# Performance work log

Hardware: AMD Instinct MI355X
Metric: run time of the kernel (lower is better)

Reference implementation:

```python
import jax, jax.numpy as jnp
import numpy as np

N, E, IN, H, C, T = 50000, 800000, 128, 64, 64, 2
F1, FO1 = H, H // T   # conv1: per-tower in/out feats
F2, FO2 = H, C // T   # conv2
STD_EPS = 1e-5
BN_EPS = 1e-5


def setup_inputs() -> dict:
    key = jax.random.key(0)
    ks = jax.random.split(key, 12)
    rn = lambda k, s, sc=0.05: jax.random.normal(k, s, jnp.float32) * sc
    return {
        "x": jax.random.normal(ks[0], (N, IN), jnp.float32),
        "embed_W": rn(ks[1], (IN, H)),
        "embed_b": jnp.zeros((H,), jnp.float32),
        "pre_W1": rn(ks[2], (T, 2 * F1, F1)),
        "pre_b1": jnp.zeros((T, F1), jnp.float32),
        "post_W1": rn(ks[3], (T, 13 * F1, FO1)),
        "post_b1": jnp.zeros((T, FO1), jnp.float32),
        "lin_W1": rn(ks[4], (H, H)),
        "lin_b1": jnp.zeros((H,), jnp.float32),
        "bn_gamma": jnp.ones((H,), jnp.float32),
        "bn_beta": jnp.zeros((H,), jnp.float32),
        "pre_W2": rn(ks[5], (T, 2 * F2, F2)),
        "pre_b2": jnp.zeros((T, F2), jnp.float32),
        "post_W2": rn(ks[6], (T, 13 * F2, FO2)),
        "post_b2": jnp.zeros((T, FO2), jnp.float32),
        "lin_W2": rn(ks[7], (C, C)),
        "lin_b2": jnp.zeros((C,), jnp.float32),
        "src": jax.random.randint(ks[8], (E,), 0, N, jnp.int32),
        "dst": jax.random.randint(ks[9], (E,), 0, N, jnp.int32),
    }


def _pna_conv(h, src, dst, deg_raw, degc, avg_log, preW, preb, postW, postb, linW, linb):
    # h: [N, F] node feats; messages flow src -> dst, aggregated at dst.
    m = jnp.concatenate([h[dst], h[src]], axis=-1)            # [E, 2F]  (cat[x_i, x_j])
    m = jnp.einsum('ef,tfg->etg', m, preW) + preb[None]       # [E, T, F] per-tower pre-NN
    seg = lambda v: jax.ops.segment_sum(v, dst, num_segments=N)
    cnt = degc[:, None, None]                                 # clamped degree >= 1
    has = (deg_raw > 0)[:, None, None]
    mean = seg(m) / cnt                                       # [N, T, F]
    mean_sq = seg(m * m) / cnt
    mn = jnp.where(has, jax.ops.segment_min(m, dst, num_segments=N), 0.0)
    mx = jnp.where(has, jax.ops.segment_max(m, dst, num_segments=N), 0.0)
    std = jnp.sqrt(jax.nn.relu(mean_sq - mean * mean) + STD_EPS)
    agg = jnp.concatenate([mean, mn, mx, std], axis=-1)       # [N, T, 4F]
    ld = jnp.log(degc + 1.0)[:, None, None]
    out = jnp.concatenate([agg, agg * (ld / avg_log), agg * (avg_log / ld)], axis=-1)  # [N, T, 12F]
    F = h.shape[-1]
    out = jnp.concatenate([jnp.broadcast_to(h[:, None, :], (N, T, F)), out], axis=-1)  # [N, T, 13F]
    out = jnp.einsum('ntf,tfg->ntg', out, postW) + postb[None]  # [N, T, FO] per-tower post-NN
    return out.reshape(N, -1) @ linW + linb                    # final mixing Linear(out, out)


def reference(x, embed_W, embed_b, pre_W1, pre_b1, post_W1, post_b1, lin_W1, lin_b1,
              bn_gamma, bn_beta, pre_W2, pre_b2, post_W2, post_b2, lin_W2, lin_b2,
              src, dst):
    deg_raw = jax.ops.segment_sum(jnp.ones((E,), jnp.float32), dst, num_segments=N)
    degc = jnp.maximum(deg_raw, 1.0)
    avg_log = jnp.mean(jnp.log(deg_raw + 1.0))  # avg_deg['log'] from the graph's degrees
    h = x @ embed_W + embed_b
    h = _pna_conv(h, src, dst, deg_raw, degc, avg_log,
                  pre_W1, pre_b1, post_W1, post_b1, lin_W1, lin_b1)
    mu = jnp.mean(h, axis=0)
    var = jnp.mean((h - mu) ** 2, axis=0)
    h = bn_gamma * (h - mu) / jnp.sqrt(var + BN_EPS) + bn_beta
    h = jax.nn.relu(h)  # dropout is identity in eval mode
    return _pna_conv(h, src, dst, deg_raw, degc, avg_log,
                     pre_W2, pre_b2, post_W2, post_b2, lin_W2, lin_b2)
```

## Files before the change

### kernel.cpp

```cpp
#include <hip/hip_runtime.h>

#define N_NODES 50000
#define E_EDGES 800000
#define IN_F    128
#define H_F     64
#define STD_EPS 1e-5f
#define BN_EPS  1e-5f

__global__ __launch_bounds__(256) void k_hist(const int* __restrict__ dst,
                                              int* __restrict__ deg) {
  int e = blockIdx.x * 256 + threadIdx.x;
  if (e < E_EDGES) atomicAdd(&deg[dst[e]], 1);
}

__global__ __launch_bounds__(256) void k_sumlog(const int* __restrict__ deg,
                                                float* __restrict__ scalars) {
  __shared__ float red[256];
  int i = blockIdx.x * 256 + threadIdx.x;
  float v = 0.f;
  if (i < N_NODES) v = logf((float)deg[i] + 1.0f);
  red[threadIdx.x] = v; __syncthreads();
  for (int s = 128; s > 0; s >>= 1) {
    if (threadIdx.x < s) red[threadIdx.x] += red[threadIdx.x + s];
    __syncthreads();
  }
  if (threadIdx.x == 0) atomicAdd(&scalars[0], red[0]);
}

__global__ __launch_bounds__(256) void k_scan_part(const int* __restrict__ deg,
                                                   int* __restrict__ partials) {
  __shared__ int red[256];
  int base = blockIdx.x * 1024;
  int s = 0;
  for (int j = threadIdx.x; j < 1024; j += 256) {
    int i = base + j;
    if (i < N_NODES) s += deg[i];
  }
  red[threadIdx.x] = s; __syncthreads();
  for (int st = 128; st > 0; st >>= 1) {
    if (threadIdx.x < st) red[threadIdx.x] += red[threadIdx.x + st];
    __syncthreads();
  }
  if (threadIdx.x == 0) partials[blockIdx.x] = red[0];
}

__global__ void k_scan_mid(int* __restrict__ partials, int nblk,
                           float* __restrict__ scalars) {
  if (threadIdx.x == 0) {
    int run = 0;
    for (int b = 0; b < nblk; b++) { int v = partials[b]; partials[b] = run; run += v; }
    scalars[1] = scalars[0] / (float)N_NODES;
  }
}

__global__ __launch_bounds__(256) void k_scan_final(const int* __restrict__ deg,
                                                    const int* __restrict__ partials,
                                                    int* __restrict__ row_ptr,
                                                    int* __restrict__ cursor) {
  __shared__ int ts[256];
  int base = blockIdx.x * 1024 + threadIdx.x * 4;
  int d[4]; int s = 0;
#pragma unroll
  for (int j = 0; j < 4; j++) {
    int i = base + j;
    d[j] = (i < N_NODES) ? deg[i] : 0;
    s += d[j];
  }
  ts[threadIdx.x] = s; __syncthreads();
  for (int off = 1; off < 256; off <<= 1) {
    int t = (threadIdx.x >= off) ? ts[threadIdx.x - off] : 0;
    __syncthreads();
    ts[threadIdx.x] += t;
    __syncthreads();
  }
  int excl = (threadIdx.x > 0) ? ts[threadIdx.x - 1] : 0;
  int run = partials[blockIdx.x] + excl;
#pragma unroll
  for (int j = 0; j < 4; j++) {
    int i = base + j;
    if (i < N_NODES) { row_ptr[i] = run; cursor[i] = run; run += d[j]; }
  }
  if (blockIdx.x == 0 && threadIdx.x == 0) row_ptr[N_NODES] = E_EDGES;
}

__global__ __launch_bounds__(256) void k_scatter(const int* __restrict__ src,
                                                 const int* __restrict__ dst,
                                                 int* __restrict__ cursor,
                                                 int* __restrict__ csr_src) {
  int e = blockIdx.x * 256 + threadIdx.x;
  if (e < E_EDGES) {
    int d = dst[e];
    int p = atomicAdd(&cursor[d], 1);
    csr_src[p] = src[e];
  }
}

__global__ __launch_bounds__(256) void k_embed(const float* __restrict__ x,
                                               const float* __restrict__ W,
                                               const float* __restrict__ bias,
                                               float* __restrict__ h) {
  __shared__ float sW[IN_F * 64];
  __shared__ float sx[IN_F * 20];
  for (int i = threadIdx.x; i < IN_F * 64; i += 256) sW[i] = W[i];
  int j = threadIdx.x & 63, ng = threadIdx.x >> 6;
  float bj = bias[j];
  for (int grp = blockIdx.x; grp < N_NODES / 16; grp += gridDim.x) {
    int n0 = grp * 16;
    __syncthreads();
    for (int idx = threadIdx.x; idx < 16 * IN_F; idx += 256) {
      int nl = idx >> 7, k = idx & 127;
      sx[k * 20 + nl] = x[(size_t)(n0 + nl) * IN_F + k];
    }
    __syncthreads();
    float a0 = bj, a1 = bj, a2 = bj, a3 = bj;
    const float* xp = &sx[ng * 4];
#pragma unroll 4
    for (int k = 0; k < IN_F; k++) {
      float4 xv = *(const float4*)&xp[k * 20];
      float w = sW[k * 64 + j];
      a0 = fmaf(xv.x, w, a0); a1 = fmaf(xv.y, w, a1);
      a2 = fmaf(xv.z, w, a2); a3 = fmaf(xv.w, w, a3);
    }
    size_t ob = (size_t)(n0 + ng * 4) * 64 + j;
    h[ob] = a0; h[ob + 64] = a1; h[ob + 128] = a2; h[ob + 192] = a3;
  }
}

template <bool BN>
__global__ __launch_bounds__(256) void k_preab(const float* __restrict__ hin,
                                               const float* __restrict__ preW,
                                               const float* __restrict__ preb,
                                               const float* __restrict__ bnscale,
                                               const float* __restrict__ bnshift,
                                               float* __restrict__ h2out,
                                               float* __restrict__ hA,
                                               float* __restrict__ hB) {
  __shared__ float sW[128 * 64];
  __shared__ float sh[64 * 20];
  int t = blockIdx.x & 1;
  const float* Wsrc = preW + (size_t)t * 128 * 64;
  for (int i = threadIdx.x; i < 128 * 64; i += 256) sW[i] = Wsrc[i];
  int f = threadIdx.x & 63, ng = threadIdx.x >> 6;
  float pb = preb[t * 64 + f];
  const float* wA = &sW[f];
  const float* wB = &sW[64 * 64 + f];
  int nblk2 = gridDim.x >> 1;
  for (int grp = blockIdx.x >> 1; grp < N_NODES / 16; grp += nblk2) {
    int n0 = grp * 16;
    __syncthreads();
    for (int idx = threadIdx.x; idx < 16 * 64; idx += 256) {
      int nl = idx >> 6, k = idx & 63;
      float v = hin[(size_t)(n0 + nl) * 64 + k];
      if (BN) {
        v = fmaxf(fmaf(v, bnscale[k], bnshift[k]), 0.f);
        if (t == 0) h2out[(size_t)(n0 + nl) * 64 + k] = v;
      }
      sh[k * 20 + nl] = v;
    }
    __syncthreads();
    float a0 = pb, a1 = pb, a2 = pb, a3 = pb;
    float b0 = 0, b1 = 0, b2 = 0, b3 = 0;
    const float* hp = &sh[ng * 4];
#pragma unroll 4
    for (int k = 0; k < 64; k++) {
      float4 hv = *(const float4*)&hp[k * 20];
      float wa = wA[k * 64], wb = wB[k * 64];
      a0 = fmaf(hv.x, wa, a0); a1 = fmaf(hv.y, wa, a1);
      a2 = fmaf(hv.z, wa, a2); a3 = fmaf(hv.w, wa, a3);
      b0 = fmaf(hv.x, wb, b0); b1 = fmaf(hv.y, wb, b1);
      b2 = fmaf(hv.z, wb, b2); b3 = fmaf(hv.w, wb, b3);
    }
    size_t nb = (size_t)(n0 + ng * 4);
    int tf = t * 64 + f;
    hA[nb * 128 + tf] = a0;          hB[nb * 128 + tf] = b0;
    hA[(nb + 1) * 128 + tf] = a1;    hB[(nb + 1) * 128 + tf] = b1;
    hA[(nb + 2) * 128 + tf] = a2;    hB[(nb + 2) * 128 + tf] = b2;
    hA[(nb + 3) * 128 + tf] = a3;    hB[(nb + 3) * 128 + tf] = b3;
  }
}

__global__ __launch_bounds__(256, 6) void k_conv(const float* __restrict__ hA,
                                                 const float* __restrict__ hB,
                                                 const float* __restrict__ hskip,
                                                 const int* __restrict__ row_ptr,
                                                 const int* __restrict__ csr_src,
                                                 const float* __restrict__ postW,
                                                 const float* __restrict__ postb,
                                                 const float* __restrict__ linW,
                                                 const float* __restrict__ linb,
                                                 const float* __restrict__ scalars,
                                                 float* __restrict__ out) {
  __shared__ float sm[2 * 5 * 8 * 64];
  __shared__ float sAB[16];
  int w = threadIdx.x >> 6, lane = threadIdx.x & 63;
  int n0 = blockIdx.x * 8;
  int t = lane >> 5, fb = (lane & 31) * 2;
  int off = t * 64 + fb;
  float avg = scalars[1];

#pragma unroll 1
  for (int k = 0; k < 2; k++) {
    int nl = w * 2 + k;
    int n = n0 + nl;
    float2 a = *(const float2*)&hA[(size_t)n * 128 + off];
    int rp0 = __builtin_amdgcn_readfirstlane(row_ptr[n]);
    int rp1 = __builtin_amdgcn_readfirstlane(row_ptr[n + 1]);
    float sx0=0,sy0=0,qx0=0,qy0=0, sx1=0,sy1=0,qx1=0,qy1=0;
    float mnx0=INFINITY,mny0=INFINITY,mxx0=-INFINITY,mxy0=-INFINITY;
    float mnx1=INFINITY,mny1=INFINITY,mxx1=-INFINITY,mxy1=-INFINITY;
    int i = rp0;
    int end4 = rp0 + ((rp1 - rp0) & ~3);
    if (i < end4) {
      int s0 = csr_src[i], s1 = csr_src[i+1], s2 = csr_src[i+2], s3 = csr_src[i+3];
      while (true) {
        float2 v0 = *(const float2*)&hB[(size_t)s0 * 128 + off];
        float2 v1 = *(const float2*)&hB[(size_t)s1 * 128 + off];
        float2 v2 = *(const float2*)&hB[(size_t)s2 * 128 + off];
        float2 v3 = *(const float2*)&hB[(size_t)s3 * 128 + off];
        i += 4;
        bool more = (i < end4);
        if (more) { s0 = csr_src[i]; s1 = csr_src[i+1]; s2 = csr_src[i+2]; s3 = csr_src[i+3]; }
        float e0x = v0.x + a.x, e0y = v0.y + a.y;
        float e1x = v1.x + a.x, e1y = v1.y + a.y;
        float e2x = v2.x + a.x, e2y = v2.y + a.y;
        float e3x = v3.x + a.x, e3y = v3.y + a.y;
        sx0 += e0x; qx0 = fmaf(e0x,e0x,qx0); mnx0 = fminf(mnx0,e0x); mxx0 = fmaxf(mxx0,e0x);
        sy0 += e0y; qy0 = fmaf(e0y,e0y,qy0); mny0 = fminf(mny0,e0y); mxy0 = fmaxf(mxy0,e0y);
        sx1 += e1x; qx1 = fmaf(e1x,e1x,qx1); mnx1 = fminf(mnx1,e1x); mxx1 = fmaxf(mxx1,e1x);
        sy1 += e1y; qy1 = fmaf(e1y,e1y,qy1); mny1 = fminf(mny1,e1y); mxy1 = fmaxf(mxy1,e1y);
        sx0 += e2x; qx0 = fmaf(e2x,e2x,qx0); mnx0 = fminf(mnx0,e2x); mxx0 = fmaxf(mxx0,e2x);
        sy0 += e2y; qy0 = fmaf(e2y,e2y,qy0); mny0 = fminf(mny0,e2y); mxy0 = fmaxf(mxy0,e2y);
        sx1 += e3x; qx1 = fmaf(e3x,e3x,qx1); mnx1 = fminf(mnx1,e3x); mxx1 = fmaxf(mxx1,e3x);
        sy1 += e3y; qy1 = fmaf(e3y,e3y,qy1); mny1 = fminf(mny1,e3y); mxy1 = fmaxf(mxy1,e3y);
        if (!more) break;
      }
    }
    {
      int r = rp1 - i;
      if (r > 0) {
        int e1i = (r > 1) ? i + 1 : i;
        int e2i = (r > 2) ? i + 2 : i;
        int t0 = csr_src[i], t1 = csr_src[e1i], t2 = csr_src[e2i];
        float2 u0 = *(const float2*)&hB[(size_t)t0 * 128 + off];
        float2 u1 = *(const float2*)&hB[(size_t)t1 * 128 + off];
        float2 u2 = *(const float2*)&hB[(size_t)t2 * 128 + off];
        float ex = u0.x + a.x, ey = u0.y + a.y;
        sx0 += ex; qx0 = fmaf(ex,ex,qx0); mnx0 = fminf(mnx0,ex); mxx0 = fmaxf(mxx0,ex);
        sy0 += ey; qy0 = fmaf(ey,ey,qy0); mny0 = fminf(mny0,ey); mxy0 = fmaxf(mxy0,ey);
        if (r > 1) {
          ex = u1.x + a.x; ey = u1.y + a.y;
          sx1 += ex; qx1 = fmaf(ex,ex,qx1); mnx1 = fminf(mnx1,ex); mxx1 = fmaxf(mxx1,ex);
          sy1 += ey; qy1 = fmaf(ey,ey,qy1); mny1 = fminf(mny1,ey); mxy1 = fmaxf(mxy1,ey);
        }
        if (r > 2) {
          ex = u2.x + a.x; ey = u2.y + a.y;
          sx0 += ex; qx0 = fmaf(ex,ex,qx0); mnx0 = fminf(mnx0,ex); mxx0 = fmaxf(mxx0,ex);
          sy0 += ey; qy0 = fmaf(ey,ey,qy0); mny0 = fminf(mny0,ey); mxy0 = fmaxf(mxy0,ey);
        }
      }
    }
    int dg = rp1 - rp0;
    float cnt = (float)(dg > 0 ? dg : 1);
    float inv = 1.0f / cnt;
    float meanx = (sx0 + sx1) * inv, meany = (sy0 + sy1) * inv;
    float qx = qx0 + qx1, qy = qy0 + qy1;
    float sdx = sqrtf(fmaxf(qx * inv - meanx * meanx, 0.f) + STD_EPS);
    float sdy = sqrtf(fmaxf(qy * inv - meany * meany, 0.f) + STD_EPS);
    float mnx = fminf(mnx0, mnx1), mny = fminf(mny0, mny1);
    float mxx = fmaxf(mxx0, mxx1), mxy = fmaxf(mxy0, mxy1);
    if (dg == 0) { mnx = 0; mny = 0; mxx = 0; mxy = 0; }
    float ldv = logf(cnt + 1.f);
    float2 hsv = *(const float2*)&hskip[(size_t)n * 64 + fb];
    float* bp = &sm[t * 2560 + nl * 64 + fb];
    *(float2*)&bp[0]    = hsv;
    *(float2*)&bp[512]  = make_float2(meanx, meany);
    *(float2*)&bp[1024] = make_float2(mnx, mny);
    *(float2*)&bp[1536] = make_float2(mxx, mxy);
    *(float2*)&bp[2048] = make_float2(sdx, sdy);
    if (lane == 0) { sAB[nl] = ldv / avg; sAB[8 + nl] = avg / ldv; }
  }
  __syncthreads();

  float g1[8] = {0,0,0,0,0,0,0,0};
  float g2[8] = {0,0,0,0,0,0,0,0};
  float g3[8] = {0,0,0,0,0,0,0,0};
  {
    int g = lane & 31, hf0 = w * 16;
    const float* pw = &postW[(size_t)t * (832 * 32) + g];
    const float* vb = &sm[t * 2560 + hf0];
#pragma unroll
    for (int j = 0; j < 16; j += 4) {
      int f13 = hf0 + j;
      float w0 = pw[f13 * 32],       w1 = pw[(f13 + 1) * 32];
      float w2 = pw[(f13 + 2) * 32], w3 = pw[(f13 + 3) * 32];
#pragma unroll
      for (int nn = 0; nn < 8; nn++) {
        float4 v = *(const float4*)&vb[nn * 64 + j];
        g1[nn] = fmaf(v.w, w3, fmaf(v.z, w2, fmaf(v.y, w1, fmaf(v.x, w0, g1[nn]))));
      }
    }
#pragma unroll
    for (int fa = 0; fa < 4; fa++) {
      const float* vfa = &vb[(1 + fa) * 512];
#pragma unroll
      for (int j = 0; j < 16; j += 4) {
        int f13 = 64 + fa * 64 + hf0 + j;
        float w10 = pw[f13 * 32],         w11 = pw[(f13 + 1) * 32];
        float w12 = pw[(f13 + 2) * 32],   w13 = pw[(f13 + 3) * 32];
        float w20 = pw[(f13 + 256) * 32], w21 = pw[(f13 + 257) * 32];
        float w22 = pw[(f13 + 258) * 32], w23 = pw[(f13 + 259) * 32];
        float w30 = pw[(f13 + 512) * 32], w31 = pw[(f13 + 513) * 32];
        float w32 = pw[(f13 + 514) * 32], w33 = pw[(f13 + 515) * 32];
#pragma unroll
        for (int nn = 0; nn < 8; nn++) {
          float4 v = *(const float4*)&vfa[nn * 64 + j];
          g1[nn] = fmaf(v.w, w13, fmaf(v.z, w12, fmaf(v.y, w11, fmaf(v.x, w10, g1[nn]))));
          g2[nn] = fmaf(v.w, w23, fmaf(v.z, w22, fmaf(v.y, w21, fmaf(v.x, w20, g2[nn]))));
          g3[nn] = fmaf(v.w, w33, fmaf(v.z, w32, fmaf(v.y, w31, fmaf(v.x, w30, g3[nn]))));
        }
      }
    }
  }
  float o8[8];
#pragma unroll
  for (int nn = 0; nn < 8; nn++)
    o8[nn] = fmaf(sAB[8 + nn], g3[nn], fmaf(sAB[nn], g2[nn], g1[nn]));
  __syncthreads();

  {
    int sw = (w + (lane >> 4)) & 3;
#pragma unroll
    for (int nn = 0; nn < 8; nn++)
      sm[((nn * 64 + lane) << 2) + sw] = o8[nn];
  }
  __syncthreads();

  {
#pragma unroll
    for (int r = 0; r < 2; r++) {
      int idx = r * 256 + (int)threadIdx.x;
      float4 p = *(const float4*)&sm[idx << 2];
      sm[2048 + idx] = p.x + p.y + p.z + p.w + postb[idx & 63];
    }
  }
  __syncthreads();

  {
    float acc0 = linb[lane], acc1 = acc0;
    const float* lw = linW + lane;
    const float* p0 = &sm[2048 + (w * 2) * 64];
    const float* p1 = p0 + 64;
#pragma unroll
    for (int c = 0; c < 64; c += 4) {
      float lw0 = lw[c * 64], lw1 = lw[(c + 1) * 64];
      float lw2 = lw[(c + 2) * 64], lw3 = lw[(c + 3) * 64];
      float4 pa = *(const float4*)&p0[c];
      float4 pb2 = *(const float4*)&p1[c];
      acc0 = fmaf(pa.w, lw3, fmaf(pa.z, lw2, fmaf(pa.y, lw1, fmaf(pa.x, lw0, acc0))));
      acc1 = fmaf(pb2.w, lw3, fmaf(pb2.z, lw2, fmaf(pb2.y, lw1, fmaf(pb2.x, lw0, acc1))));
    }
    size_t ob = (size_t)(n0 + w * 2) * 64 + lane;
    out[ob] = acc0;
    out[ob + 64] = acc1;
  }
}

__global__ __launch_bounds__(256) void k_bnstats(const float* __restrict__ y,
                                                 float* __restrict__ bnsum,
                                                 float* __restrict__ bnsumsq) {
  __shared__ float r1[256], r2[256];
  int c = threadIdx.x & 63, r = threadIdx.x >> 6;
  float s = 0, q = 0;
  for (int n = blockIdx.x * 4 + r; n < N_NODES; n += gridDim.x * 4) {
    float v = y[(size_t)n * 64 + c];
    s += v; q = fmaf(v, v, q);
  }
  r1[threadIdx.x] = s; r2[threadIdx.x] = q; __syncthreads();
  if (threadIdx.x < 64) {
    s = r1[threadIdx.x] + r1[threadIdx.x + 64] + r1[threadIdx.x + 128] + r1[threadIdx.x + 192];
    q = r2[threadIdx.x] + r2[threadIdx.x + 64] + r2[threadIdx.x + 128] + r2[threadIdx.x + 192];
    atomicAdd(&bnsum[threadIdx.x], s);
    atomicAdd(&bnsumsq[threadIdx.x], q);
  }
}

__global__ void k_bnfin(const float* __restrict__ bnsum, const float* __restrict__ bnsumsq,
                        const float* __restrict__ gamma, const float* __restrict__ beta,
                        float* __restrict__ bnscale, float* __restrict__ bnshift) {
  int c = threadIdx.x;
  if (c < 64) {
    float mu = bnsum[c] * (1.f / N_NODES);
    float var = bnsumsq[c] * (1.f / N_NODES) - mu * mu;
    float sc = gamma[c] / sqrtf(var + BN_EPS);
    bnscale[c] = sc;
    bnshift[c] = fmaf(-mu, sc, beta[c]);
  }
}

extern "C" void kernel_launch(void* const* d_in, const int* in_sizes, int n_in,
                              void* d_out, int out_size, void* d_ws, size_t ws_size,
                              hipStream_t stream) {
  const float* x      = (const float*)d_in[0];
  const float* embW   = (const float*)d_in[1];
  const float* embB   = (const float*)d_in[2];
  const float* preW1  = (const float*)d_in[3];
  const float* preb1  = (const float*)d_in[4];
  const float* postW1 = (const float*)d_in[5];
  const float* postb1 = (const float*)d_in[6];
  const float* linW1  = (const float*)d_in[7];
  const float* linb1  = (const float*)d_in[8];
  const float* gamma  = (const float*)d_in[9];
  const float* beta   = (const float*)d_in[10];
  const float* preW2  = (const float*)d_in[11];
  const float* preb2  = (const float*)d_in[12];
  const float* postW2 = (const float*)d_in[13];
  const float* postb2 = (const float*)d_in[14];
  const float* linW2  = (const float*)d_in[15];
  const float* linb2  = (const float*)d_in[16];
  const int*   src    = (const int*)d_in[17];
  const int*   dst    = (const int*)d_in[18];
  float* out = (float*)d_out;

  char* w = (char*)d_ws;
  size_t o = 0;
  int*   deg     = (int*)(w + o);   o += (size_t)N_NODES * 4;
  float* scalars = (float*)(w + o); o += 64;
  float* bnsum   = (float*)(w + o); o += 256;
  float* bnsumsq = (float*)(w + o); o += 256;
  float* bnscale = (float*)(w + o); o += 256;
  float* bnshift = (float*)(w + o); o += 256;
  size_t zero_len = o;
  o = (o + 255) & ~(size_t)255;
  int* partials = (int*)(w + o);  o += 256;
  int* row_ptr  = (int*)(w + o);  o += (size_t)(N_NODES + 1) * 4; o = (o + 255) & ~(size_t)255;
  int* cursor   = (int*)(w + o);  o += (size_t)N_NODES * 4;       o = (o + 255) & ~(size_t)255;
  int* csr      = (int*)(w + o);  o += (size_t)E_EDGES * 4;       o = (o + 255) & ~(size_t)255;
  float* h1 = (float*)(w + o); o += (size_t)N_NODES * 64 * 4;
  float* y1 = (float*)(w + o); o += (size_t)N_NODES * 64 * 4;
  float* h2 = (float*)(w + o); o += (size_t)N_NODES * 64 * 4;
  float* hA = (float*)(w + o); o += (size_t)N_NODES * 128 * 4;
  float* hB = (float*)(w + o); o += (size_t)N_NODES * 128 * 4;

  hipMemsetAsync(w, 0, zero_len, stream);

  const int NBLK_SCAN = (N_NODES + 1023) / 1024;
  k_hist<<<(E_EDGES + 255) / 256, 256, 0, stream>>>(dst, deg);
  k_sumlog<<<(N_NODES + 255) / 256, 256, 0, stream>>>(deg, scalars);
  k_scan_part<<<NBLK_SCAN, 256, 0, stream>>>(deg, partials);
  k_scan_mid<<<1, 64, 0, stream>>>(partials, NBLK_SCAN, scalars);
  k_scan_final<<<NBLK_SCAN, 256, 0, stream>>>(deg, partials, row_ptr, cursor);
  k_scatter<<<(E_EDGES + 255) / 256, 256, 0, stream>>>(src, dst, cursor, csr);

  k_embed<<<768, 256, 0, stream>>>(x, embW, embB, h1);

  k_preab<false><<<1024, 256, 0, stream>>>(h1, preW1, preb1, nullptr, nullptr, nullptr, hA, hB);
  k_conv<<<N_NODES / 8, 256, 0, stream>>>(hA, hB, h1, row_ptr, csr,
                                          postW1, postb1, linW1, linb1, scalars, y1);
  k_bnstats<<<256, 256, 0, stream>>>(y1, bnsum, bnsumsq);
  k_bnfin<<<1, 64, 0, stream>>>(bnsum, bnsumsq, gamma, beta, bnscale, bnshift);

  k_preab<true><<<1024, 256, 0, stream>>>(y1, preW2, preb2, bnscale, bnshift, h2, hA, hB);
  k_conv<<<N_NODES / 8, 256, 0, stream>>>(hA, hB, h2, row_ptr, csr,
                                          postW2, postb2, linW2, linb2, scalars, out);
}
```

Baseline: 580.8 us.

## Enlarge node tiles in pre-NN and conv kernels for more weight reuse

The pre-NN kernel now computes 8 nodes per thread instead of 4, with a 32-node tile, and stores the A/B weight halves interleaved so one float2 load fetches both. The conv kernel handles 16 nodes per block instead of 8, so each postW and linW weight load is reused across twice as many nodes. The per-node degree scale factors are now recomputed from row_ptr in the epilogue instead of being kept in shared memory. The aim is to cut redundant weight loads, at the cost of more registers and lower occupancy (launch bounds drop from 6 to 4), plus fewer blocks for the latency-bound gather phase.

```diff
diff --git a/kernel.cpp b/kernel.cpp
--- a/kernel.cpp
+++ b/kernel.cpp
@@ -135,51 +135,68 @@
                                                float* __restrict__ h2out,
                                                float* __restrict__ hA,
                                                float* __restrict__ hB) {
-  __shared__ float sW[128 * 64];
-  __shared__ float sh[64 * 20];
+  __shared__ float sWp[64 * 128];
+  __shared__ float sh[64 * 36];
   int t = blockIdx.x & 1;
   const float* Wsrc = preW + (size_t)t * 128 * 64;
-  for (int i = threadIdx.x; i < 128 * 64; i += 256) sW[i] = Wsrc[i];
+  for (int i = threadIdx.x; i < 64 * 64; i += 256) {
+    int k = i >> 6, f = i & 63;
+    float wa = Wsrc[k * 64 + f];
+    float wb = Wsrc[(64 + k) * 64 + f];
+    *(float2*)&sWp[k * 128 + f * 2] = make_float2(wa, wb);
+  }
   int f = threadIdx.x & 63, ng = threadIdx.x >> 6;
   float pb = preb[t * 64 + f];
-  const float* wA = &sW[f];
-  const float* wB = &sW[64 * 64 + f];
   int nblk2 = gridDim.x >> 1;
-  for (int grp = blockIdx.x >> 1; grp < N_NODES / 16; grp += nblk2) {
-    int n0 = grp * 16;
-    __syncthreads();
-    for (int idx = threadIdx.x; idx < 16 * 64; idx += 256) {
+  const int NGRP = (N_NODES + 31) / 32;
+  for (int grp = blockIdx.x >> 1; grp < NGRP; grp += nblk2) {
+    int n0 = grp * 32;
+    __syncthreads();
+    for (int idx = threadIdx.x; idx < 32 * 64; idx += 256) {
       int nl = idx >> 6, k = idx & 63;
-      float v = hin[(size_t)(n0 + nl) * 64 + k];
-      if (BN) {
-        v = fmaxf(fmaf(v, bnscale[k], bnshift[k]), 0.f);
-        if (t == 0) h2out[(size_t)(n0 + nl) * 64 + k] = v;
-      }
-      sh[k * 20 + nl] = v;
-    }
-    __syncthreads();
-    float a0 = pb, a1 = pb, a2 = pb, a3 = pb;
-    float b0 = 0, b1 = 0, b2 = 0, b3 = 0;
-    const float* hp = &sh[ng * 4];
+      int n = n0 + nl;
+      float v = 0.f;
+      if (n < N_NODES) {
+        v = hin[(size_t)n * 64 + k];
+        if (BN) {
+          v = fmaxf(fmaf(v, bnscale[k], bnshift[k]), 0.f);
+          if (t == 0) h2out[(size_t)n * 64 + k] = v;
+        }
+      }
+      sh[k * 36 + nl] = v;
+    }
+    __syncthreads();
+    float a[8] = {pb, pb, pb, pb, pb, pb, pb, pb};
+    float b[8] = {0, 0, 0, 0, 0, 0, 0, 0};
+    const float* hp = &sh[ng * 8];
+    const float* wp = &sWp[f * 2];
 #pragma unroll 4
     for (int k = 0; k < 64; k++) {
-      float4 hv = *(const float4*)&hp[k * 20];
-      float wa = wA[k * 64], wb = wB[k * 64];
-      a0 = fmaf(hv.x, wa, a0); a1 = fmaf(hv.y, wa, a1);
-      a2 = fmaf(hv.z, wa, a2); a3 = fmaf(hv.w, wa, a3);
-      b0 = fmaf(hv.x, wb, b0); b1 = fmaf(hv.y, wb, b1);
-      b2 = fmaf(hv.z, wb, b2); b3 = fmaf(hv.w, wb, b3);
-    }
-    size_t nb = (size_t)(n0 + ng * 4);
+      float4 h0 = *(const float4*)&hp[k * 36];
+      float4 h1 = *(const float4*)&hp[k * 36 + 4];
+      float2 w2 = *(const float2*)&wp[k * 128];
+      a[0] = fmaf(h0.x, w2.x, a[0]); b[0] = fmaf(h0.x, w2.y, b[0]);
+      a[1] = fmaf(h0.y, w2.x, a[1]); b[1] = fmaf(h0.y, w2.y, b[1]);
+      a[2] = fmaf(h0.z, w2.x, a[2]); b[2] = fmaf(h0.z, w2.y, b[2]);
+      a[3] = fmaf(h0.w, w2.x, a[3]); b[3] = fmaf(h0.w, w2.y, b[3]);
+      a[4] = fmaf(h1.x, w2.x, a[4]); b[4] = fmaf(h1.x, w2.y, b[4]);
+      a[5] = fmaf(h1.y, w2.x, a[5]); b[5] = fmaf(h1.y, w2.y, b[5]);
+      a[6] = fmaf(h1.z, w2.x, a[6]); b[6] = fmaf(h1.z, w2.y, b[6]);
+      a[7] = fmaf(h1.w, w2.x, a[7]); b[7] = fmaf(h1.w, w2.y, b[7]);
+    }
     int tf = t * 64 + f;
-    hA[nb * 128 + tf] = a0;          hB[nb * 128 + tf] = b0;
-    hA[(nb + 1) * 128 + tf] = a1;    hB[(nb + 1) * 128 + tf] = b1;
-    hA[(nb + 2) * 128 + tf] = a2;    hB[(nb + 2) * 128 + tf] = b2;
-    hA[(nb + 3) * 128 + tf] = a3;    hB[(nb + 3) * 128 + tf] = b3;
-  }
-}
-
-__global__ __launch_bounds__(256, 6) void k_conv(const float* __restrict__ hA,
+#pragma unroll
+    for (int j = 0; j < 8; j++) {
+      int n = n0 + ng * 8 + j;
+      if (n < N_NODES) {
+        hA[(size_t)n * 128 + tf] = a[j];
+        hB[(size_t)n * 128 + tf] = b[j];
+      }
+    }
+  }
+}
+
+__global__ __launch_bounds__(256, 4) void k_conv(const float* __restrict__ hA,
                                                  const float* __restrict__ hB,
                                                  const float* __restrict__ hskip,
                                                  const int* __restrict__ row_ptr,
@@ -190,17 +207,16 @@
                                                  const float* __restrict__ linb,
                                                  const float* __restrict__ scalars,
                                                  float* __restrict__ out) {
-  __shared__ float sm[2 * 5 * 8 * 64];
-  __shared__ float sAB[16];
+  __shared__ float sm[2 * 5 * 16 * 64];
   int w = threadIdx.x >> 6, lane = threadIdx.x & 63;
-  int n0 = blockIdx.x * 8;
+  int n0 = blockIdx.x * 16;
   int t = lane >> 5, fb = (lane & 31) * 2;
   int off = t * 64 + fb;
   float avg = scalars[1];
 
 #pragma unroll 1
-  for (int k = 0; k < 2; k++) {
-    int nl = w * 2 + k;
+  for (int kk = 0; kk < 4; kk++) {
+    int nl = w * 4 + kk;
     int n = n0 + nl;
     float2 a = *(const float2*)&hA[(size_t)n * 128 + off];
     int rp0 = __builtin_amdgcn_readfirstlane(row_ptr[n]);
@@ -269,39 +285,37 @@
     float mnx = fminf(mnx0, mnx1), mny = fminf(mny0, mny1);
     float mxx = fmaxf(mxx0, mxx1), mxy = fmaxf(mxy0, mxy1);
     if (dg == 0) { mnx = 0; mny = 0; mxx = 0; mxy = 0; }
-    float ldv = logf(cnt + 1.f);
     float2 hsv = *(const float2*)&hskip[(size_t)n * 64 + fb];
-    float* bp = &sm[t * 2560 + nl * 64 + fb];
+    float* bp = &sm[t * 5120 + nl * 64 + fb];
     *(float2*)&bp[0]    = hsv;
-    *(float2*)&bp[512]  = make_float2(meanx, meany);
-    *(float2*)&bp[1024] = make_float2(mnx, mny);
-    *(float2*)&bp[1536] = make_float2(mxx, mxy);
-    *(float2*)&bp[2048] = make_float2(sdx, sdy);
-    if (lane == 0) { sAB[nl] = ldv / avg; sAB[8 + nl] = avg / ldv; }
+    *(float2*)&bp[1024] = make_float2(meanx, meany);
+    *(float2*)&bp[2048] = make_float2(mnx, mny);
+    *(float2*)&bp[3072] = make_float2(mxx, mxy);
+    *(float2*)&bp[4096] = make_float2(sdx, sdy);
   }
   __syncthreads();
 
-  float g1[8] = {0,0,0,0,0,0,0,0};
-  float g2[8] = {0,0,0,0,0,0,0,0};
-  float g3[8] = {0,0,0,0,0,0,0,0};
+  float g1[16], g2[16], g3[16];
+#pragma unroll
+  for (int nn = 0; nn < 16; nn++) { g1[nn] = 0; g2[nn] = 0; g3[nn] = 0; }
   {
     int g = lane & 31, hf0 = w * 16;
     const float* pw = &postW[(size_t)t * (832 * 32) + g];
-    const float* vb = &sm[t * 2560 + hf0];
+    const float* vb = &sm[t * 5120 + hf0];
 #pragma unroll
     for (int j = 0; j < 16; j += 4) {
       int f13 = hf0 + j;
       float w0 = pw[f13 * 32],       w1 = pw[(f13 + 1) * 32];
       float w2 = pw[(f13 + 2) * 32], w3 = pw[(f13 + 3) * 32];
 #pragma unroll
-      for (int nn = 0; nn < 8; nn++) {
+      for (int nn = 0; nn < 16; nn++) {
         float4 v = *(const float4*)&vb[nn * 64 + j];
         g1[nn] = fmaf(v.w, w3, fmaf(v.z, w2, fmaf(v.y, w1, fmaf(v.x, w0, g1[nn]))));
       }
     }
 #pragma unroll
     for (int fa = 0; fa < 4; fa++) {
-      const float* vfa = &vb[(1 + fa) * 512];
+      const float* vfa = &vb[(1 + fa) * 1024];
 #pragma unroll
       for (int j = 0; j < 16; j += 4) {
         int f13 = 64 + fa * 64 + hf0 + j;
@@ -312,7 +326,7 @@
         float w30 = pw[(f13 + 512) * 32], w31 = pw[(f13 + 513) * 32];
         float w32 = pw[(f13 + 514) * 32], w33 = pw[(f13 + 515) * 32];
 #pragma unroll
-        for (int nn = 0; nn < 8; nn++) {
+        for (int nn = 0; nn < 16; nn++) {
           float4 v = *(const float4*)&vfa[nn * 64 + j];
           g1[nn] = fmaf(v.w, w13, fmaf(v.z, w12, fmaf(v.y, w11, fmaf(v.x, w10, g1[nn]))));
           g2[nn] = fmaf(v.w, w23, fmaf(v.z, w22, fmaf(v.y, w21, fmaf(v.x, w20, g2[nn]))));
@@ -321,47 +335,55 @@
       }
     }
   }
-  float o8[8];
-#pragma unroll
-  for (int nn = 0; nn < 8; nn++)
-    o8[nn] = fmaf(sAB[8 + nn], g3[nn], fmaf(sAB[nn], g2[nn], g1[nn]));
+  float o16[16];
+#pragma unroll
+  for (int nn = 0; nn < 16; nn++) {
+    int dgn = row_ptr[n0 + nn + 1] - row_ptr[n0 + nn];
+    float cntn = (float)(dgn > 0 ? dgn : 1);
+    float ldv = logf(cntn + 1.f);
+    float sA = ldv / avg, sB = avg / ldv;
+    o16[nn] = fmaf(sB, g3[nn], fmaf(sA, g2[nn], g1[nn]));
+  }
   __syncthreads();
 
   {
     int sw = (w + (lane >> 4)) & 3;
 #pragma unroll
-    for (int nn = 0; nn < 8; nn++)
-      sm[((nn * 64 + lane) << 2) + sw] = o8[nn];
+    for (int nn = 0; nn < 16; nn++)
+      sm[((nn * 64 + lane) << 2) + sw] = o16[nn];
   }
   __syncthreads();
 
   {
 #pragma unroll
-    for (int r = 0; r < 2; r++) {
+    for (int r = 0; r < 4; r++) {
       int idx = r * 256 + (int)threadIdx.x;
       float4 p = *(const float4*)&sm[idx << 2];
-      sm[2048 + idx] = p.x + p.y + p.z + p.w + postb[idx & 63];
+      sm[4096 + idx] = p.x + p.y + p.z + p.w + postb[idx & 63];
     }
   }
   __syncthreads();
 
   {
-    float acc0 = linb[lane], acc1 = acc0;
+    float lb = linb[lane];
+    float acc0 = lb, acc1 = lb, acc2 = lb, acc3 = lb;
     const float* lw = linW + lane;
-    const float* p0 = &sm[2048 + (w * 2) * 64];
-    const float* p1 = p0 + 64;
+    const float* p0 = &sm[4096 + (w * 4) * 64];
 #pragma unroll
     for (int c = 0; c < 64; c += 4) {
       float lw0 = lw[c * 64], lw1 = lw[(c + 1) * 64];
       float lw2 = lw[(c + 2) * 64], lw3 = lw[(c + 3) * 64];
       float4 pa = *(const float4*)&p0[c];
-      float4 pb2 = *(const float4*)&p1[c];
+      float4 pb = *(const float4*)&p0[64 + c];
+      float4 pc = *(const float4*)&p0[128 + c];
+      float4 pd = *(const float4*)&p0[192 + c];
       acc0 = fmaf(pa.w, lw3, fmaf(pa.z, lw2, fmaf(pa.y, lw1, fmaf(pa.x, lw0, acc0))));
-      acc1 = fmaf(pb2.w, lw3, fmaf(pb2.z, lw2, fmaf(pb2.y, lw1, fmaf(pb2.x, lw0, acc1))));
-    }
-    size_t ob = (size_t)(n0 + w * 2) * 64 + lane;
-    out[ob] = acc0;
-    out[ob + 64] = acc1;
+      acc1 = fmaf(pb.w, lw3, fmaf(pb.z, lw2, fmaf(pb.y, lw1, fmaf(pb.x, lw0, acc1))));
+      acc2 = fmaf(pc.w, lw3, fmaf(pc.z, lw2, fmaf(pc.y, lw1, fmaf(pc.x, lw0, acc2))));
+      acc3 = fmaf(pd.w, lw3, fmaf(pd.z, lw2, fmaf(pd.y, lw1, fmaf(pd.x, lw0, acc3))));
+    }
+    size_t ob = (size_t)(n0 + w * 4) * 64 + lane;
+    out[ob] = acc0; out[ob + 64] = acc1; out[ob + 128] = acc2; out[ob + 192] = acc3;
   }
 }
 
@@ -453,13 +475,13 @@
 
   k_embed<<<768, 256, 0, stream>>>(x, embW, embB, h1);
 
-  k_preab<false><<<1024, 256, 0, stream>>>(h1, preW1, preb1, nullptr, nullptr, nullptr, hA, hB);
-  k_conv<<<N_NODES / 8, 256, 0, stream>>>(hA, hB, h1, row_ptr, csr,
-                                          postW1, postb1, linW1, linb1, scalars, y1);
+  k_preab<false><<<768, 256, 0, stream>>>(h1, preW1, preb1, nullptr, nullptr, nullptr, hA, hB);
+  k_conv<<<N_NODES / 16, 256, 0, stream>>>(hA, hB, h1, row_ptr, csr,
+                                           postW1, postb1, linW1, linb1, scalars, y1);
   k_bnstats<<<256, 256, 0, stream>>>(y1, bnsum, bnsumsq);
   k_bnfin<<<1, 64, 0, stream>>>(bnsum, bnsumsq, gamma, beta, bnscale, bnshift);
 
-  k_preab<true><<<1024, 256, 0, stream>>>(y1, preW2, preb2, bnscale, bnshift, h2, hA, hB);
-  k_conv<<<N_NODES / 8, 256, 0, stream>>>(hA, hB, h2, row_ptr, csr,
-                                          postW2, postb2, linW2, linb2, scalars, out);
-}
+  k_preab<true><<<768, 256, 0, stream>>>(y1, preW2, preb2, bnscale, bnshift, h2, hA, hB);
+  k_conv<<<N_NODES / 16, 256, 0, stream>>>(hA, hB, h2, row_ptr, csr,
+                                           postW2, postb2, linW2, linb2, scalars, out);
+}
```

Result: no change. 574.4 us (-1.1%).
